# Performance work log

Hardware: AMD Instinct MI355X
Metric: run time of the kernel (lower is better)

Reference implementation:

```python
import jax, jax.numpy as jnp
import numpy as np

B, N, D, H = 4, 1024, 1024, 16
HD = D // H  # 64
EPS = 1e-5


def rotate_half(t):
    # unflatten last dim to (..., HD//2, 2), swap-and-negate, flatten back
    t2 = t.reshape(t.shape[:-1] + (HD // 2, 2))
    x1, x2 = t2[..., 0], t2[..., 1]
    return jnp.stack((-x2, x1), axis=-1).reshape(t.shape)


def setup_inputs() -> dict:
    key = jax.random.key(0)
    ks = jax.random.split(key, 12)
    s = 0.02
    return {
        "x": jax.random.normal(ks[0], (B, N, D), jnp.float32),
        "encoding": jax.random.uniform(ks[1], (2, B, 1, N, HD), jnp.float32),
        "Wqkv_w": jax.random.normal(ks[2], (3 * D, D), jnp.float32) * s,
        "Wqkv_b": jnp.zeros((3 * D,), jnp.float32),
        "out_w": jax.random.normal(ks[3], (D, D), jnp.float32) * s,
        "out_b": jnp.zeros((D,), jnp.float32),
        "ffn1_w": jax.random.normal(ks[4], (2 * D, 2 * D), jnp.float32) * s,
        "ffn1_b": jnp.zeros((2 * D,), jnp.float32),
        "ln_g": jnp.ones((2 * D,), jnp.float32),
        "ln_b": jnp.zeros((2 * D,), jnp.float32),
        "ffn2_w": jax.random.normal(ks[5], (D, 2 * D), jnp.float32) * s,
        "ffn2_b": jnp.zeros((D,), jnp.float32),
    }


def reference(x, encoding, Wqkv_w, Wqkv_b, out_w, out_b,
              ffn1_w, ffn1_b, ln_g, ln_b, ffn2_w, ffn2_b):
    b, n, d = x.shape
    # fused QKV projection: [B,N,3D] -> [B,H,N,HD,3]
    qkv = x @ Wqkv_w.T + Wqkv_b
    qkv = qkv.reshape(b, n, H, HD, 3).transpose(0, 2, 1, 3, 4)
    q, k, v = qkv[..., 0], qkv[..., 1], qkv[..., 2]
    # cached rotary embedding: t*cos + rotate_half(t)*sin
    q = q * encoding[0] + rotate_half(q) * encoding[1]
    k = k * encoding[0] + rotate_half(k) * encoding[1]
    # scaled dot-product attention (mask is None in this path)
    scale = HD ** -0.5
    sim = jnp.einsum('bhid,bhjd->bhij', q, k) * scale
    attn = jax.nn.softmax(sim, axis=-1)
    ctx = jnp.einsum('bhij,bhjd->bhid', attn, v)
    ctx = ctx.transpose(0, 2, 1, 3).reshape(b, n, d)
    message = ctx @ out_w.T + out_b
    # FFN on concat([x, message]) with interposed LayerNorm + GELU (exact)
    h = jnp.concatenate([x, message], axis=-1) @ ffn1_w.T + ffn1_b
    mu = h.mean(-1, keepdims=True)
    var = ((h - mu) ** 2).mean(-1, keepdims=True)
    h = (h - mu) * jax.lax.rsqrt(var + EPS) * ln_g + ln_b
    h = jax.nn.gelu(h, approximate=False)
    return x + h @ ffn2_w.T + ffn2_b
```

## Files before the change

kernel.cpp:

```cpp
#include <hip/hip_runtime.h>
#include <hip/hip_bf16.h>
#include <math.h>

#define B_ 4
#define N_ 1024
#define D_ 1024
#define H_ 16
#define HD_ 64
#define M_ (B_*N_)

typedef __hip_bfloat16 bf16;
using floatx4 = __attribute__((ext_vector_type(4))) float;
using shortx8 = __attribute__((ext_vector_type(8))) short;

__device__ __forceinline__ float to_f(bf16 v) { return __bfloat162float(v); }
__device__ __forceinline__ float s2f(short v) {
    unsigned u = ((unsigned)(unsigned short)v) << 16;
    return __builtin_bit_cast(float, u);
}
__device__ __forceinline__ short bf_s(float x) {
    bf16 h = __float2bfloat16(x);
    return *reinterpret_cast<short*>(&h);
}

#define GLOBAL_AS __attribute__((address_space(1)))
#define LDS_AS    __attribute__((address_space(3)))
__device__ __forceinline__ void load_lds16(const void* g, void* l) {
    __builtin_amdgcn_global_load_lds((const GLOBAL_AS unsigned int*)g,
                                     (LDS_AS unsigned int*)l, 16, 0, 0);
}

__device__ __forceinline__ void storec(float* p, float v) { *p = v; }
__device__ __forceinline__ void storec(bf16*  p, float v) { *p = __float2bfloat16(v); }

template<typename TC, bool RESID, bool SPLIT, int BN>
__global__ __launch_bounds__(256)
void mgemm(const bf16* __restrict__ A, int lda,
           const bf16* __restrict__ A2, int lda2, int K1,
           const bf16* __restrict__ W, int ldw,
           const float* __restrict__ bias,
           const float* __restrict__ resid, int ldr,
           TC* __restrict__ C, int ldc,
           int M, int N, int K)
{
    constexpr int NT  = BN / 32;
    constexpr int ASZ = 128 * 32;
    constexpr int BSZ = BN * 32;
    __shared__ short lds[2 * (ASZ + BSZ)];

    int t = threadIdx.x;
    int lane = t & 63, quad = lane >> 4, l15 = lane & 15;
    int wave = t >> 6, wm = wave & 1, wn = wave >> 1;

    int gx = gridDim.x;
    int bid = blockIdx.y * gx + blockIdx.x;
    int seg = bid / (8 * gx);
    int rem = bid - seg * 8 * gx;
    int bx = rem >> 3;
    int by = seg * 8 + (rem & 7);
    int row0 = by * 128, col0 = bx * BN;

    const short* Ag  = (const short*)A;
    const short* A2g = (const short*)A2;
    const short* Wg  = (const short*)W;

    auto stage = [&](int buf, int k0) {
        short* As = lds + buf * (ASZ + BSZ);
        short* Bs = As + ASZ;
        #pragma unroll
        for (int pass = 0; pass < 2; ++pass) {
            int idx = pass * 256 + t;
            int r = idx >> 2, c8 = (idx & 3) << 3;
            int wub = (pass * 256 + (t & 192)) * 8;
            const short* asrc;
            if (SPLIT && k0 >= K1)
                asrc = A2g + (size_t)(row0 + r) * lda2 + (k0 - K1) + c8;
            else
                asrc = Ag + (size_t)(row0 + r) * lda + k0 + c8;
            load_lds16(asrc, &As[wub]);
        }
        #pragma unroll
        for (int pass = 0; pass < BN / 64; ++pass) {
            int idx = pass * 256 + t;
            int r = idx >> 2, c8 = (idx & 3) << 3;
            int wub = (pass * 256 + (t & 192)) * 8;
            load_lds16(Wg + (size_t)(col0 + r) * ldw + k0 + c8, &Bs[wub]);
        }
    };

    floatx4 acc[4][NT];
    #pragma unroll
    for (int mt = 0; mt < 4; ++mt)
        #pragma unroll
        for (int nt = 0; nt < NT; ++nt)
            acc[mt][nt] = (floatx4){0.f, 0.f, 0.f, 0.f};

    stage(0, 0);
    int buf = 0;
    for (int k0 = 0; k0 < K; k0 += 32, buf ^= 1) {
        __syncthreads();
        const short* As = lds + buf * (ASZ + BSZ);
        const short* Bs = As + ASZ;
        shortx8 af[4], bfv[NT];
        #pragma unroll
        for (int mt = 0; mt < 4; ++mt)
            af[mt] = *(const shortx8*)&As[(wm * 64 + mt * 16 + l15) * 32 + quad * 8];
        #pragma unroll
        for (int nt = 0; nt < NT; ++nt)
            bfv[nt] = *(const shortx8*)&Bs[(wn * (BN / 2) + nt * 16 + l15) * 32 + quad * 8];
        if (k0 + 32 < K) stage(buf ^ 1, k0 + 32);
        #pragma unroll
        for (int mt = 0; mt < 4; ++mt)
            #pragma unroll
            for (int nt = 0; nt < NT; ++nt)
                acc[mt][nt] = __builtin_amdgcn_mfma_f32_16x16x32_bf16(
                    af[mt], bfv[nt], acc[mt][nt], 0, 0, 0);
    }

    #pragma unroll
    for (int mt = 0; mt < 4; ++mt) {
        #pragma unroll
        for (int nt = 0; nt < NT; ++nt) {
            int col = col0 + wn * (BN / 2) + nt * 16 + l15;
            float bv = bias[col];
            #pragma unroll
            for (int r = 0; r < 4; ++r) {
                int row = row0 + wm * 64 + mt * 16 + quad * 4 + r;
                float v = acc[mt][nt][r] + bv;
                if (RESID) v += resid[(size_t)row * ldr + col];
                storec(&C[(size_t)row * ldc + col], v);
            }
        }
    }
}

__global__ void f2b_all(const float* __restrict__ s0, bf16* __restrict__ d0,
                        const float* __restrict__ s1, bf16* __restrict__ d1,
                        const float* __restrict__ s2, bf16* __restrict__ d2,
                        const float* __restrict__ s3, bf16* __restrict__ d3,
                        const float* __restrict__ s4, bf16* __restrict__ d4)
{
    int blk = blockIdx.x;
    const float* s; bf16* d; int base;
    if      (blk < 4096)  { s = s0; d = d0; base = blk; }
    else if (blk < 7168)  { s = s1; d = d1; base = blk - 4096; }
    else if (blk < 8192)  { s = s2; d = d2; base = blk - 7168; }
    else if (blk < 12288) { s = s3; d = d3; base = blk - 8192; }
    else                  { s = s4; d = d4; base = blk - 12288; }
    int i = base * 1024 + threadIdx.x * 4;
    float4 v = *(const float4*)&s[i];
    d[i + 0] = __float2bfloat16(v.x);
    d[i + 1] = __float2bfloat16(v.y);
    d[i + 2] = __float2bfloat16(v.z);
    d[i + 3] = __float2bfloat16(v.w);
}

#define RS 196
__global__ __launch_bounds__(256)
void rope_all(const bf16* __restrict__ qkv, const float* __restrict__ enc,
              bf16* __restrict__ q, bf16* __restrict__ k, bf16* __restrict__ vt)
{
    __shared__ short raw[64 * RS];
    int n0 = blockIdx.x * 64, h = blockIdx.y, b = blockIdx.z;
    int t = threadIdx.x;
    const short* qg = (const short*)qkv;

    {
        int row = t >> 2, off = (t & 3) * 48;
        const short* src = qg + ((size_t)(b * N_ + n0 + row)) * 3072 + h * 192 + off;
        uint4 u[3];
        u[0] = ((const uint4*)src)[0];
        u[1] = ((const uint4*)src)[1];
        u[2] = ((const uint4*)src)[2];
        uint4 u2[3];
        u2[0] = ((const uint4*)src)[3];
        u2[1] = ((const uint4*)src)[4];
        u2[2] = ((const uint4*)src)[5];
        uint2* dst = (uint2*)&raw[row * RS + off];
        const uint2* p = (const uint2*)u;
        #pragma unroll
        for (int i = 0; i < 6; ++i) dst[i] = p[i];
        const uint2* p2 = (const uint2*)u2;
        #pragma unroll
        for (int i = 0; i < 6; ++i) dst[6 + i] = p2[i];
    }
    __syncthreads();

    size_t bh = (size_t)(b * H_ + h);
    {
        int d = t & 63, g0 = t >> 6;
        int dp = d ^ 1;
        float sgn = (d & 1) ? 1.0f : -1.0f;
        #pragma unroll
        for (int i = 0; i < 16; ++i) {
            int nl = g0 + 4 * i;
            const short* r = &raw[nl * RS];
            float qv = s2f(r[3 * d]),  kv = s2f(r[3 * d + 1]);
            float qp = s2f(r[3 * dp]), kp = s2f(r[3 * dp + 1]);
            size_t ei = ((size_t)(b * N_ + n0 + nl)) * HD_ + d;
            float c = enc[ei];
            float s = enc[(size_t)B_ * N_ * HD_ + ei];
            size_t o = (bh * N_ + n0 + nl) * HD_ + d;
            q[o] = __float2bfloat16(qv * c + sgn * qp * s);
            k[o] = __float2bfloat16(kv * c + sgn * kp * s);
        }
    }
    {
        int nl = t & 63, g0 = t >> 6;
        #pragma unroll
        for (int i = 0; i < 16; ++i) {
            int dt = g0 + 4 * i;
            vt[(bh * HD_ + dt) * N_ + n0 + nl] =
                *reinterpret_cast<bf16*>(&raw[nl * RS + 3 * dt + 2]);
        }
    }
}

__global__ __launch_bounds__(256, 2)
void fattn(const bf16* __restrict__ q, const bf16* __restrict__ k,
           const bf16* __restrict__ vt, bf16* __restrict__ ctx)
{
    const int i0 = blockIdx.x * 128;
    const int h = blockIdx.y, b = blockIdx.z;
    const int t = threadIdx.x;
    const int lane = t & 63;
    const int w = t >> 6;
    const int quad = lane >> 4, l15 = lane & 15;

    __shared__ alignas(16) short Ks[64 * 72];
    __shared__ alignas(16) short Vs[64 * 72];
    __shared__ alignas(16) short Ps[128 * 72];

    const size_t bh = (size_t)(b * H_ + h) * N_;
    const size_t bhv = (size_t)(b * H_ + h) * HD_;
    const short* qg = (const short*)q;
    const short* kg = (const short*)k;
    const short* vg = (const short*)vt;

    shortx8 qf[2][2];
    #pragma unroll
    for (int rt = 0; rt < 2; ++rt) {
        const short* qrow = qg + (bh + i0 + w * 32 + rt * 16 + l15) * HD_;
        qf[rt][0] = *(const shortx8*)(qrow + quad * 8);
        qf[rt][1] = *(const shortx8*)(qrow + 32 + quad * 8);
    }

    floatx4 O[2][4];
    #pragma unroll
    for (int rt = 0; rt < 2; ++rt)
        #pragma unroll
        for (int dt = 0; dt < 4; ++dt) O[rt][dt] = (floatx4){0.f, 0.f, 0.f, 0.f};
    float lsum[2][4] = {};

    const int srow = t >> 2, soff = (t & 3) * 16;

    for (int j0 = 0; j0 < N_; j0 += 64) {
        __syncthreads();
        {
            const uint4* src = (const uint4*)(kg + (bh + j0 + srow) * HD_ + soff);
            uint4 a0 = src[0], a1 = src[1];
            *(uint4*)&Ks[srow * 72 + soff]     = a0;
            *(uint4*)&Ks[srow * 72 + soff + 8] = a1;
        }
        {
            const uint4* src = (const uint4*)(vg + (bhv + srow) * N_ + j0 + soff);
            uint4 a0 = src[0], a1 = src[1];
            *(uint4*)&Vs[srow * 72 + soff]     = a0;
            *(uint4*)&Vs[srow * 72 + soff + 8] = a1;
        }
        __syncthreads();

        floatx4 S[2][4];
        #pragma unroll
        for (int rt = 0; rt < 2; ++rt)
            #pragma unroll
            for (int ct = 0; ct < 4; ++ct) S[rt][ct] = (floatx4){0.f, 0.f, 0.f, 0.f};
        #pragma unroll
        for (int ct = 0; ct < 4; ++ct) {
            shortx8 b0 = *(const shortx8*)&Ks[(ct * 16 + l15) * 72 + quad * 8];
            shortx8 b1 = *(const shortx8*)&Ks[(ct * 16 + l15) * 72 + 32 + quad * 8];
            #pragma unroll
            for (int rt = 0; rt < 2; ++rt) {
                S[rt][ct] = __builtin_amdgcn_mfma_f32_16x16x32_bf16(qf[rt][0], b0, S[rt][ct], 0, 0, 0);
                S[rt][ct] = __builtin_amdgcn_mfma_f32_16x16x32_bf16(qf[rt][1], b1, S[rt][ct], 0, 0, 0);
            }
        }

        #pragma unroll
        for (int rt = 0; rt < 2; ++rt)
            #pragma unroll
            for (int ct = 0; ct < 4; ++ct)
                #pragma unroll
                for (int r = 0; r < 4; ++r) {
                    float e = __expf(S[rt][ct][r] * 0.125f);
                    lsum[rt][r] += e;
                    Ps[(w * 32 + rt * 16 + quad * 4 + r) * 72 + ct * 16 + l15] = bf_s(e);
                }

        shortx8 pa[2][2];
        #pragma unroll
        for (int rt = 0; rt < 2; ++rt) {
            pa[rt][0] = *(const shortx8*)&Ps[(w * 32 + rt * 16 + l15) * 72 + quad * 8];
            pa[rt][1] = *(const shortx8*)&Ps[(w * 32 + rt * 16 + l15) * 72 + 32 + quad * 8];
        }
        #pragma unroll
        for (int dt = 0; dt < 4; ++dt) {
            shortx8 vb0 = *(const shortx8*)&Vs[(dt * 16 + l15) * 72 + quad * 8];
            shortx8 vb1 = *(const shortx8*)&Vs[(dt * 16 + l15) * 72 + 32 + quad * 8];
            #pragma unroll
            for (int rt = 0; rt < 2; ++rt) {
                O[rt][dt] = __builtin_amdgcn_mfma_f32_16x16x32_bf16(pa[rt][0], vb0, O[rt][dt], 0, 0, 0);
                O[rt][dt] = __builtin_amdgcn_mfma_f32_16x16x32_bf16(pa[rt][1], vb1, O[rt][dt], 0, 0, 0);
            }
        }
    }

    #pragma unroll
    for (int rt = 0; rt < 2; ++rt)
        #pragma unroll
        for (int r = 0; r < 4; ++r) {
            float rs = lsum[rt][r];
            #pragma unroll
            for (int msk = 1; msk < 16; msk <<= 1)
                rs += __shfl_xor(rs, msk);
            float inv = 1.0f / rs;
            int row = i0 + w * 32 + rt * 16 + quad * 4 + r;
            #pragma unroll
            for (int dt = 0; dt < 4; ++dt)
                ctx[((size_t)(b * N_ + row)) * D_ + h * HD_ + dt * 16 + l15] =
                    __float2bfloat16(O[rt][dt][r] * inv);
        }
}

__global__ void ln_gelu(bf16* __restrict__ hbuf, const float* __restrict__ g,
                        const float* __restrict__ beta)
{
    int row = blockIdx.x;
    int t = threadIdx.x;
    bf16* hr = hbuf + (size_t)row * 2048;
    float vals[8];
    float s = 0.f, s2 = 0.f;
    #pragma unroll
    for (int l = 0; l < 8; ++l) {
        float x = to_f(hr[t + 256 * l]);
        vals[l] = x; s += x; s2 += x * x;
    }
    __shared__ float rs[256], rs2[256];
    rs[t] = s; rs2[t] = s2; __syncthreads();
    for (int k2 = 128; k2 > 0; k2 >>= 1) {
        if (t < k2) { rs[t] += rs[t + k2]; rs2[t] += rs2[t + k2]; }
        __syncthreads();
    }
    float mu  = rs[0] * (1.0f / 2048.0f);
    float var = rs2[0] * (1.0f / 2048.0f) - mu * mu;
    float rstd = rsqrtf(var + 1e-5f);
    #pragma unroll
    for (int l = 0; l < 8; ++l) {
        int c = t + 256 * l;
        float xn = (vals[l] - mu) * rstd * g[c] + beta[c];
        hr[c] = __float2bfloat16(0.5f * xn * (1.0f + erff(xn * 0.70710678118654752f)));
    }
}

extern "C" void kernel_launch(void* const* d_in, const int* in_sizes, int n_in,
                              void* d_out, int out_size, void* d_ws, size_t ws_size,
                              hipStream_t stream)
{
    const float* x      = (const float*)d_in[0];
    const float* enc    = (const float*)d_in[1];
    const float* Wqkv_w = (const float*)d_in[2];
    const float* Wqkv_b = (const float*)d_in[3];
    const float* out_w  = (const float*)d_in[4];
    const float* out_b  = (const float*)d_in[5];
    const float* ffn1_w = (const float*)d_in[6];
    const float* ffn1_b = (const float*)d_in[7];
    const float* ln_g   = (const float*)d_in[8];
    const float* ln_b   = (const float*)d_in[9];
    const float* ffn2_w = (const float*)d_in[10];
    const float* ffn2_b = (const float*)d_in[11];
    float* out = (float*)d_out;

    float* ws = (float*)d_ws;
    bf16* qkv16 = (bf16*)ws;
    bf16* ctx16 = (bf16*)ws;
    bf16* h16   = (bf16*)(ws + 2097152);
    bf16* q16   = (bf16*)(ws + 6291456);
    bf16* k16   = q16 + 2097152;
    bf16* vt16  = k16 + 2097152;
    bf16* msg16 = (bf16*)(ws + 6291456);
    bf16* x16   = (bf16*)(ws + 12582912);
    bf16* wq16  = (bf16*)(ws + 14680064);
    bf16* wo16  = wq16 + 3145728;
    bf16* wf1   = wo16 + 1048576;
    bf16* wf2   = wf1 + 4194304;

    f2b_all<<<14336, 256, 0, stream>>>(x, x16, Wqkv_w, wq16, out_w, wo16,
                                       ffn1_w, wf1, ffn2_w, wf2);

    dim3 g1(3072 / 128, 4096 / 128);
    mgemm<bf16, false, false, 128><<<g1, 256, 0, stream>>>(
        x16, 1024, nullptr, 0, 0, wq16, 1024, Wqkv_b, nullptr, 0,
        qkv16, 3072, 4096, 3072, 1024);

    dim3 gr(16, 16, 4);
    rope_all<<<gr, 256, 0, stream>>>(qkv16, enc, q16, k16, vt16);

    dim3 ga(N_ / 128, H_, B_);
    fattn<<<ga, 256, 0, stream>>>(q16, k16, vt16, ctx16);

    dim3 g2(1024 / 64, 4096 / 128);
    mgemm<bf16, false, false, 64><<<g2, 256, 0, stream>>>(
        ctx16, 1024, nullptr, 0, 0, wo16, 1024, out_b, nullptr, 0,
        msg16, 1024, 4096, 1024, 1024);

    dim3 g3(2048 / 128, 4096 / 128);
    mgemm<bf16, false, true, 128><<<g3, 256, 0, stream>>>(
        x16, 1024, msg16, 1024, 1024, wf1, 2048, ffn1_b, nullptr, 0,
        h16, 2048, 4096, 2048, 2048);

    ln_gelu<<<4096, 256, 0, stream>>>(h16, ln_g, ln_b);

    dim3 g4(1024 / 64, 4096 / 128);
    mgemm<float, true, false, 64><<<g4, 256, 0, stream>>>(
        h16, 2048, nullptr, 0, 0, wf2, 2048, ffn2_b, x, 1024,
        out, 1024, 4096, 1024, 2048);
}
```

Baseline: 299.9 us.

## Fuse rotary embedding and Q/K/V scatter into QKV GEMM epilogue

Removes the separate rope_all kernel and the intermediate qkv buffer. Wqkv rows and bias are permuted during the bf16 conversion so that output columns group as Q, K and V sections. The QKV GEMM epilogue then applies rotary (pairing neighbours with a lane shuffle) and writes q, k and transposed v straight to their final layouts. This saves one launch and a full write-plus-read of the QKV tensor, at the cost of scattered uncoalesced stores, especially the strided V-transpose writes, and per-element encoding loads inside the GEMM.

```diff
diff --git a/kernel.cpp b/kernel.cpp
--- a/kernel.cpp
+++ b/kernel.cpp
@@ -33,7 +33,7 @@
 __device__ __forceinline__ void storec(float* p, float v) { *p = v; }
 __device__ __forceinline__ void storec(bf16*  p, float v) { *p = __float2bfloat16(v); }
 
-template<typename TC, bool RESID, bool SPLIT, int BN>
+template<typename TC, bool RESID, bool SPLIT, int BN, bool QKV>
 __global__ __launch_bounds__(256)
 void mgemm(const bf16* __restrict__ A, int lda,
            const bf16* __restrict__ A2, int lda2, int K1,
@@ -41,6 +41,8 @@
            const float* __restrict__ bias,
            const float* __restrict__ resid, int ldr,
            TC* __restrict__ C, int ldc,
+           bf16* __restrict__ qd, bf16* __restrict__ kd, bf16* __restrict__ vtd,
+           const float* __restrict__ enc,
            int M, int N, int K)
 {
     constexpr int NT  = BN / 32;
@@ -117,6 +119,40 @@
                     af[mt], bfv[nt], acc[mt][nt], 0, 0, 0);
     }
 
+    if (QKV) {
+        int sec = col0 >> 10;
+        #pragma unroll
+        for (int mt = 0; mt < 4; ++mt) {
+            #pragma unroll
+            for (int nt = 0; nt < NT; ++nt) {
+                int col = col0 + wn * (BN / 2) + nt * 16 + l15;
+                int cl = col & 1023, h = cl >> 6, d = cl & 63;
+                float bv = bias[col];
+                float sgn = (d & 1) ? 1.0f : -1.0f;
+                #pragma unroll
+                for (int r = 0; r < 4; ++r) {
+                    int row = row0 + wm * 64 + mt * 16 + quad * 4 + r;
+                    int b = row >> 10, n = row & 1023;
+                    float val = acc[mt][nt][r] + bv;
+                    if (sec < 2) {
+                        float pair = __shfl_xor(val, 1);
+                        size_t ei = ((size_t)(b * N_ + n)) * HD_ + d;
+                        float cv = enc[ei];
+                        float sv = enc[(size_t)B_ * N_ * HD_ + ei];
+                        float ro = val * cv + sgn * pair * sv;
+                        size_t o = (((size_t)(b * H_ + h)) * N_ + n) * HD_ + d;
+                        if (sec == 0) qd[o] = __float2bfloat16(ro);
+                        else          kd[o] = __float2bfloat16(ro);
+                    } else {
+                        vtd[(((size_t)(b * H_ + h)) * HD_ + d) * N_ + n] =
+                            __float2bfloat16(val);
+                    }
+                }
+            }
+        }
+        return;
+    }
+
     #pragma unroll
     for (int mt = 0; mt < 4; ++mt) {
         #pragma unroll
@@ -138,82 +174,37 @@
                         const float* __restrict__ s1, bf16* __restrict__ d1,
                         const float* __restrict__ s2, bf16* __restrict__ d2,
                         const float* __restrict__ s3, bf16* __restrict__ d3,
-                        const float* __restrict__ s4, bf16* __restrict__ d4)
+                        const float* __restrict__ wqkv, bf16* __restrict__ wq,
+                        const float* __restrict__ bq, float* __restrict__ bqp)
 {
     int blk = blockIdx.x;
+    if (blk >= 11264) {
+        int j = blk - 11264;
+        int sec = j >> 10, rr = j & 1023;
+        int h = rr >> 6, d = rr & 63;
+        int src = h * 192 + d * 3 + sec;
+        const float* sp = wqkv + (size_t)src * 1024;
+        bf16* dp = wq + (size_t)j * 1024;
+        int i = threadIdx.x * 4;
+        float4 v = *(const float4*)&sp[i];
+        dp[i + 0] = __float2bfloat16(v.x);
+        dp[i + 1] = __float2bfloat16(v.y);
+        dp[i + 2] = __float2bfloat16(v.z);
+        dp[i + 3] = __float2bfloat16(v.w);
+        if (threadIdx.x == 0) bqp[j] = bq[src];
+        return;
+    }
     const float* s; bf16* d; int base;
     if      (blk < 4096)  { s = s0; d = d0; base = blk; }
-    else if (blk < 7168)  { s = s1; d = d1; base = blk - 4096; }
-    else if (blk < 8192)  { s = s2; d = d2; base = blk - 7168; }
-    else if (blk < 12288) { s = s3; d = d3; base = blk - 8192; }
-    else                  { s = s4; d = d4; base = blk - 12288; }
+    else if (blk < 5120)  { s = s1; d = d1; base = blk - 4096; }
+    else if (blk < 9216)  { s = s2; d = d2; base = blk - 5120; }
+    else                  { s = s3; d = d3; base = blk - 9216; }
     int i = base * 1024 + threadIdx.x * 4;
     float4 v = *(const float4*)&s[i];
     d[i + 0] = __float2bfloat16(v.x);
     d[i + 1] = __float2bfloat16(v.y);
     d[i + 2] = __float2bfloat16(v.z);
     d[i + 3] = __float2bfloat16(v.w);
-}
-
-#define RS 196
-__global__ __launch_bounds__(256)
-void rope_all(const bf16* __restrict__ qkv, const float* __restrict__ enc,
-              bf16* __restrict__ q, bf16* __restrict__ k, bf16* __restrict__ vt)
-{
-    __shared__ short raw[64 * RS];
-    int n0 = blockIdx.x * 64, h = blockIdx.y, b = blockIdx.z;
-    int t = threadIdx.x;
-    const short* qg = (const short*)qkv;
-
-    {
-        int row = t >> 2, off = (t & 3) * 48;
-        const short* src = qg + ((size_t)(b * N_ + n0 + row)) * 3072 + h * 192 + off;
-        uint4 u[3];
-        u[0] = ((const uint4*)src)[0];
-        u[1] = ((const uint4*)src)[1];
-        u[2] = ((const uint4*)src)[2];
-        uint4 u2[3];
-        u2[0] = ((const uint4*)src)[3];
-        u2[1] = ((const uint4*)src)[4];
-        u2[2] = ((const uint4*)src)[5];
-        uint2* dst = (uint2*)&raw[row * RS + off];
-        const uint2* p = (const uint2*)u;
-        #pragma unroll
-        for (int i = 0; i < 6; ++i) dst[i] = p[i];
-        const uint2* p2 = (const uint2*)u2;
-        #pragma unroll
-        for (int i = 0; i < 6; ++i) dst[6 + i] = p2[i];
-    }
-    __syncthreads();
-
-    size_t bh = (size_t)(b * H_ + h);
-    {
-        int d = t & 63, g0 = t >> 6;
-        int dp = d ^ 1;
-        float sgn = (d & 1) ? 1.0f : -1.0f;
-        #pragma unroll
-        for (int i = 0; i < 16; ++i) {
-            int nl = g0 + 4 * i;
-            const short* r = &raw[nl * RS];
-            float qv = s2f(r[3 * d]),  kv = s2f(r[3 * d + 1]);
-            float qp = s2f(r[3 * dp]), kp = s2f(r[3 * dp + 1]);
-            size_t ei = ((size_t)(b * N_ + n0 + nl)) * HD_ + d;
-            float c = enc[ei];
-            float s = enc[(size_t)B_ * N_ * HD_ + ei];
-            size_t o = (bh * N_ + n0 + nl) * HD_ + d;
-            q[o] = __float2bfloat16(qv * c + sgn * qp * s);
-            k[o] = __float2bfloat16(kv * c + sgn * kp * s);
-        }
-    }
-    {
-        int nl = t & 63, g0 = t >> 6;
-        #pragma unroll
-        for (int i = 0; i < 16; ++i) {
-            int dt = g0 + 4 * i;
-            vt[(bh * HD_ + dt) * N_ + n0 + nl] =
-                *reinterpret_cast<bf16*>(&raw[nl * RS + 3 * dt + 2]);
-        }
-    }
 }
 
 __global__ __launch_bounds__(256, 2)
@@ -381,7 +372,6 @@
     float* out = (float*)d_out;
 
     float* ws = (float*)d_ws;
-    bf16* qkv16 = (bf16*)ws;
     bf16* ctx16 = (bf16*)ws;
     bf16* h16   = (bf16*)(ws + 2097152);
     bf16* q16   = (bf16*)(ws + 6291456);
@@ -393,35 +383,33 @@
     bf16* wo16  = wq16 + 3145728;
     bf16* wf1   = wo16 + 1048576;
     bf16* wf2   = wf1 + 4194304;
-
-    f2b_all<<<14336, 256, 0, stream>>>(x, x16, Wqkv_w, wq16, out_w, wo16,
-                                       ffn1_w, wf1, ffn2_w, wf2);
+    float* qkvb = ws + 19922944;
+
+    f2b_all<<<14336, 256, 0, stream>>>(x, x16, out_w, wo16, ffn1_w, wf1,
+                                       ffn2_w, wf2, Wqkv_w, wq16, Wqkv_b, qkvb);
 
     dim3 g1(3072 / 128, 4096 / 128);
-    mgemm<bf16, false, false, 128><<<g1, 256, 0, stream>>>(
-        x16, 1024, nullptr, 0, 0, wq16, 1024, Wqkv_b, nullptr, 0,
-        qkv16, 3072, 4096, 3072, 1024);
-
-    dim3 gr(16, 16, 4);
-    rope_all<<<gr, 256, 0, stream>>>(qkv16, enc, q16, k16, vt16);
+    mgemm<bf16, false, false, 128, true><<<g1, 256, 0, stream>>>(
+        x16, 1024, nullptr, 0, 0, wq16, 1024, qkvb, nullptr, 0,
+        (bf16*)nullptr, 0, q16, k16, vt16, enc, 4096, 3072, 1024);
 
     dim3 ga(N_ / 128, H_, B_);
     fattn<<<ga, 256, 0, stream>>>(q16, k16, vt16, ctx16);
 
     dim3 g2(1024 / 64, 4096 / 128);
-    mgemm<bf16, false, false, 64><<<g2, 256, 0, stream>>>(
+    mgemm<bf16, false, false, 64, false><<<g2, 256, 0, stream>>>(
         ctx16, 1024, nullptr, 0, 0, wo16, 1024, out_b, nullptr, 0,
-        msg16, 1024, 4096, 1024, 1024);
+        msg16, 1024, nullptr, nullptr, nullptr, nullptr, 4096, 1024, 1024);
 
     dim3 g3(2048 / 128, 4096 / 128);
-    mgemm<bf16, false, true, 128><<<g3, 256, 0, stream>>>(
+    mgemm<bf16, false, true, 128, false><<<g3, 256, 0, stream>>>(
         x16, 1024, msg16, 1024, 1024, wf1, 2048, ffn1_b, nullptr, 0,
-        h16, 2048, 4096, 2048, 2048);
+        h16, 2048, nullptr, nullptr, nullptr, nullptr, 4096, 2048, 2048);
 
     ln_gelu<<<4096, 256, 0, stream>>>(h16, ln_g, ln_b);
 
     dim3 g4(1024 / 64, 4096 / 128);
-    mgemm<float, true, false, 64><<<g4, 256, 0, stream>>>(
+    mgemm<float, true, false, 64, false><<<g4, 256, 0, stream>>>(
         h16, 2048, nullptr, 0, 0, wf2, 2048, ffn2_b, x, 1024,
-        out, 1024, 4096, 1024, 2048);
-}
+        out, 1024, nullptr, nullptr, nullptr, nullptr, 4096, 1024, 2048);
+}
```

Result: slower. 314.2 us (+4.8%).
